# Kernel tuning notes

Hardware: AMD Instinct MI355X
Metric: run time of the kernel (lower is better)

Reference implementation:

```python
import jax, jax.numpy as jnp
import numpy as np


def setup_inputs() -> dict:
    key = jax.random.key(0)
    ks = jax.random.split(key, 5)
    B, C, H, W = 16, 512, 32, 32
    n_heads, d_k = 4, 128
    return {
        "x": jax.random.normal(ks[0], (B, C, H, W), dtype=jnp.float32),
        "w_proj": jax.random.normal(ks[1], (3 * n_heads * d_k, C), dtype=jnp.float32) * (1.0 / np.sqrt(C)),
        "b_proj": jax.random.normal(ks[2], (3 * n_heads * d_k,), dtype=jnp.float32) * 0.01,
        "w_out": jax.random.normal(ks[3], (C, n_heads * d_k), dtype=jnp.float32) * (1.0 / np.sqrt(n_heads * d_k)),
        "b_out": jax.random.normal(ks[4], (C,), dtype=jnp.float32) * 0.01,
        "n_heads": n_heads,
    }


def reference(x, w_proj, b_proj, w_out, b_out, n_heads):
    B, C, H, W = x.shape
    seq = H * W
    d_k = (w_proj.shape[0] // 3) // n_heads
    scale = d_k ** -0.5

    xs = x.reshape(B, C, seq).transpose(0, 2, 1)          # [B, seq, C]
    qkv = xs @ w_proj.T + b_proj                           # [B, seq, 3*H*d_k]
    qkv = qkv.reshape(B, seq, n_heads, 3 * d_k)
    q, k, v = jnp.split(qkv, 3, axis=-1)                   # each [B, seq, H, d_k]

    attn = jnp.einsum('bihd,bjhd->bijh', q, k) * scale     # [B, seq, seq, H]
    # NOTE: softmax over the QUERY axis (dim=1), faithful to the source quirk.
    attn = jax.nn.softmax(attn, axis=1)

    res = jnp.einsum('bijh,bjhd->bihd', attn, v)           # [B, seq, H, d_k]
    res = res.reshape(B, seq, n_heads * d_k)
    res = res @ w_out.T + b_out + xs                       # residual add
    return res.transpose(0, 2, 1).reshape(B, C, H, W)
```

## Files before the change

kernel.cpp:

```cpp
#include <hip/hip_runtime.h>
#include <hip/hip_bf16.h>
#include <math.h>

#define B_    16
#define CIN   512
#define SEQ   1024
#define NH    4
#define DK    128
#define OUT3  1536
#define SCALE 0.08838834764831845f

typedef __attribute__((ext_vector_type(8))) __bf16 bf16x8;
typedef __attribute__((ext_vector_type(4))) float f32x4;

#define MFMA(a, b, c) __builtin_amdgcn_mfma_f32_16x16x32_bf16((a), (b), (c), 0, 0, 0)

__device__ __forceinline__ ushort f2bf(float f) {
    __hip_bfloat16 h = __float2bfloat16(f);
    return *(ushort*)&h;
}
__device__ __forceinline__ uint pk2(float a, float b) {
    return (uint)f2bf(a) | ((uint)f2bf(b) << 16);
}

__global__ __launch_bounds__(256) void transpose_cast_kernel(
    const float* __restrict__ x, ushort* __restrict__ xt)
{
    __shared__ ushort t[64 * 66];
    const int tid = threadIdx.x;
    const int i0 = blockIdx.x * 64, c0 = blockIdx.y * 64, b = blockIdx.z;

    #pragma unroll
    for (int l = 0; l < 4; ++l) {
        int idx = tid + l * 256;
        int c = idx >> 4, i4 = (idx & 15) << 2;
        float4 v = *(const float4*)&x[((size_t)b * CIN + c0 + c) * SEQ + i0 + i4];
        t[(i4 + 0) * 66 + c] = f2bf(v.x);
        t[(i4 + 1) * 66 + c] = f2bf(v.y);
        t[(i4 + 2) * 66 + c] = f2bf(v.z);
        t[(i4 + 3) * 66 + c] = f2bf(v.w);
    }
    __syncthreads();
    #pragma unroll
    for (int l = 0; l < 4; ++l) {
        int idx = tid + l * 256;
        int i = idx >> 4, c4 = (idx & 15) << 2;
        uint2 p;
        p.x = *(const uint*)&t[i * 66 + c4];
        p.y = *(const uint*)&t[i * 66 + c4 + 2];
        *(uint2*)&xt[((size_t)b * SEQ + i0 + i) * CIN + c0 + c4] = p;
    }
}

__global__ __launch_bounds__(256) void qkv_kernel(
    const float* __restrict__ w, const float* __restrict__ bias,
    const ushort* __restrict__ xt,
    ushort* __restrict__ qb, ushort* __restrict__ kb, ushort* __restrict__ vtb)
{
    __shared__ ushort lds_w[128 * 40];
    __shared__ ushort lds_x[128 * 40];
    const int tid = threadIdx.x;
    const int lane = tid & 63, wv = tid >> 6;
    const int l15 = lane & 15, l4 = lane >> 4;
    const int wm = wv >> 1, wn = wv & 1;
    const int o0 = blockIdx.x * 128, i0 = blockIdx.y * 128, b = blockIdx.z;

    f32x4 acc[4][4] = {};
    for (int c0 = 0; c0 < CIN; c0 += 32) {
        __syncthreads();
        #pragma unroll
        for (int l = 0; l < 4; ++l) {
            int idx = tid + l * 256;
            int o = idx >> 3, cq = (idx & 7) << 2;
            float4 v = *(const float4*)&w[(size_t)(o0 + o) * CIN + c0 + cq];
            uint2 p; p.x = pk2(v.x, v.y); p.y = pk2(v.z, v.w);
            *(uint2*)&lds_w[o * 40 + cq] = p;
        }
        #pragma unroll
        for (int l = 0; l < 2; ++l) {
            int idx = tid + l * 256;
            int i = idx >> 2, cq = (idx & 3) << 3;
            *(uint4*)&lds_x[i * 40 + cq] =
                *(const uint4*)&xt[((size_t)b * SEQ + i0 + i) * CIN + c0 + cq];
        }
        __syncthreads();
        bf16x8 af[4], bfr[4];
        #pragma unroll
        for (int m = 0; m < 4; ++m)
            af[m] = *(const bf16x8*)&lds_w[(wm * 64 + m * 16 + l15) * 40 + (l4 << 3)];
        #pragma unroll
        for (int n = 0; n < 4; ++n)
            bfr[n] = *(const bf16x8*)&lds_x[(wn * 64 + n * 16 + l15) * 40 + (l4 << 3)];
        #pragma unroll
        for (int m = 0; m < 4; ++m)
            #pragma unroll
            for (int n = 0; n < 4; ++n)
                acc[m][n] = MFMA(af[m], bfr[n], acc[m][n]);
    }
    const int h = o0 / 384, which = (o0 % 384) / 128;
    const int bh = b * NH + h;
    #pragma unroll
    for (int m = 0; m < 4; ++m) {
        const int d0 = wm * 64 + m * 16 + (l4 << 2);
        float bia[4];
        #pragma unroll
        for (int r = 0; r < 4; ++r) bia[r] = bias[o0 + d0 + r];
        #pragma unroll
        for (int n = 0; n < 4; ++n) {
            const int i = i0 + wn * 64 + n * 16 + l15;
            float v0 = acc[m][n][0] + bia[0], v1 = acc[m][n][1] + bia[1];
            float v2 = acc[m][n][2] + bia[2], v3 = acc[m][n][3] + bia[3];
            if (which == 2) {
                vtb[((size_t)bh * DK + d0 + 0) * SEQ + i] = f2bf(v0);
                vtb[((size_t)bh * DK + d0 + 1) * SEQ + i] = f2bf(v1);
                vtb[((size_t)bh * DK + d0 + 2) * SEQ + i] = f2bf(v2);
                vtb[((size_t)bh * DK + d0 + 3) * SEQ + i] = f2bf(v3);
            } else {
                ushort* dst = (which == 0) ? qb : kb;
                uint2 p; p.x = pk2(v0, v1); p.y = pk2(v2, v3);
                *(uint2*)&dst[((size_t)bh * SEQ + i) * DK + d0] = p;
            }
        }
    }
}

__global__ __launch_bounds__(256) void stats_kernel(
    const ushort* __restrict__ qb, const ushort* __restrict__ kb,
    float* __restrict__ mstat, float* __restrict__ rstat)
{
    __shared__ ushort lds_q[64 * 136];
    const int tid = threadIdx.x;
    const int lane = tid & 63, wv = tid >> 6;
    const int l15 = lane & 15, l4 = lane >> 4;
    const int bh = blockIdx.y;
    const int j0 = blockIdx.x * 128 + wv * 32;
    const ushort* kbase = kb + (size_t)bh * SEQ * DK;
    const ushort* qbase = qb + (size_t)bh * SEQ * DK;

    bf16x8 kf[2][4];
    #pragma unroll
    for (int m = 0; m < 2; ++m)
        #pragma unroll
        for (int ks = 0; ks < 4; ++ks)
            kf[m][ks] = *(const bf16x8*)&kbase[(size_t)(j0 + m * 16 + l15) * DK
                                               + ks * 32 + (l4 << 3)];
    float mm[2][4], ss[2][4];
    #pragma unroll
    for (int m = 0; m < 2; ++m)
        #pragma unroll
        for (int r = 0; r < 4; ++r) { mm[m][r] = -1e30f; ss[m][r] = 0.0f; }

    for (int it = 0; it < SEQ / 64; ++it) {
        __syncthreads();
        #pragma unroll
        for (int l = 0; l < 4; ++l) {
            int idx = tid + l * 256;
            int i = idx >> 4, dq = (idx & 15) << 3;
            *(uint4*)&lds_q[i * 136 + dq] =
                *(const uint4*)&qbase[(size_t)(it * 64 + i) * DK + dq];
        }
        __syncthreads();
        #pragma unroll
        for (int n = 0; n < 4; ++n) {
            f32x4 a0 = {}, a1 = {};
            #pragma unroll
            for (int ks = 0; ks < 4; ++ks) {
                bf16x8 bq = *(const bf16x8*)&lds_q[(n * 16 + l15) * 136
                                                   + ks * 32 + (l4 << 3)];
                a0 = MFMA(kf[0][ks], bq, a0);
                a1 = MFMA(kf[1][ks], bq, a1);
            }
            #pragma unroll
            for (int r = 0; r < 4; ++r) {
                float v0 = a0[r] * SCALE;
                float n0 = fmaxf(mm[0][r], v0);
                ss[0][r] = ss[0][r] * __expf(mm[0][r] - n0) + __expf(v0 - n0);
                mm[0][r] = n0;
                float v1 = a1[r] * SCALE;
                float n1 = fmaxf(mm[1][r], v1);
                ss[1][r] = ss[1][r] * __expf(mm[1][r] - n1) + __expf(v1 - n1);
                mm[1][r] = n1;
            }
        }
    }
    #pragma unroll
    for (int m = 0; m < 2; ++m)
        #pragma unroll
        for (int r = 0; r < 4; ++r) {
            float mv = mm[m][r], sv = ss[m][r];
            #pragma unroll
            for (int wmask = 1; wmask < 16; wmask <<= 1) {
                float mo = __shfl_xor(mv, wmask, 64);
                float so = __shfl_xor(sv, wmask, 64);
                float mn = fmaxf(mv, mo);
                sv = sv * __expf(mv - mn) + so * __expf(mo - mn);
                mv = mn;
            }
            if (l15 == 0) {
                int j = j0 + m * 16 + (l4 << 2) + r;
                mstat[(size_t)bh * SEQ + j] = mv;
                rstat[(size_t)bh * SEQ + j] = 1.0f / sv;
            }
        }
}

__global__ __launch_bounds__(256) void attn_kernel(
    const ushort* __restrict__ qb, const ushort* __restrict__ kb,
    const ushort* __restrict__ vtb,
    const float* __restrict__ mstat, const float* __restrict__ rstat,
    ushort* __restrict__ resb)
{
    __shared__ ushort lds_k[64 * 136];
    __shared__ ushort lds_vt[128 * 72];
    __shared__ ushort lds_p[64 * 72];
    const int tid = threadIdx.x;
    const int lane = tid & 63, wv = tid >> 6;
    const int l15 = lane & 15, l4 = lane >> 4;
    const int wj = wv & 1, wi = wv >> 1;
    const int bh = blockIdx.y, b = bh >> 2, h = bh & 3;
    const int i0 = blockIdx.x * 64;
    const ushort* qbase = qb + (size_t)bh * SEQ * DK;
    const ushort* kbase = kb + (size_t)bh * SEQ * DK;
    const ushort* vtbase = vtb + (size_t)bh * DK * SEQ;

    bf16x8 qf[2][4];
    #pragma unroll
    for (int n = 0; n < 2; ++n)
        #pragma unroll
        for (int ks = 0; ks < 4; ++ks)
            qf[n][ks] = *(const bf16x8*)&qbase[(size_t)(i0 + wi * 32 + n * 16 + l15) * DK
                                               + ks * 32 + (l4 << 3)];
    f32x4 oacc[2][4] = {};

    for (int jt = 0; jt < SEQ / 64; ++jt) {
        const int j0 = jt * 64;
        __syncthreads();
        #pragma unroll
        for (int l = 0; l < 4; ++l) {
            int idx = tid + l * 256;
            int j = idx >> 4, dq = (idx & 15) << 3;
            *(uint4*)&lds_k[j * 136 + dq] =
                *(const uint4*)&kbase[(size_t)(j0 + j) * DK + dq];
        }
        #pragma unroll
        for (int l = 0; l < 4; ++l) {
            int idx = tid + l * 256;
            int d = idx >> 3, jq = (idx & 7) << 3;
            *(uint4*)&lds_vt[d * 72 + jq] =
                *(const uint4*)&vtbase[(size_t)d * SEQ + j0 + jq];
        }
        __syncthreads();
        float mj[2][4], rj[2][4];
        #pragma unroll
        for (int m = 0; m < 2; ++m)
            #pragma unroll
            for (int r = 0; r < 4; ++r) {
                int j = j0 + wj * 32 + m * 16 + (l4 << 2) + r;
                mj[m][r] = mstat[(size_t)bh * SEQ + j];
                rj[m][r] = rstat[(size_t)bh * SEQ + j];
            }
        bf16x8 af[2][4];
        #pragma unroll
        for (int m = 0; m < 2; ++m)
            #pragma unroll
            for (int ks = 0; ks < 4; ++ks)
                af[m][ks] = *(const bf16x8*)&lds_k[(wj * 32 + m * 16 + l15) * 136
                                                   + ks * 32 + (l4 << 3)];
        #pragma unroll
        for (int m = 0; m < 2; ++m)
            #pragma unroll
            for (int n = 0; n < 2; ++n) {
                f32x4 s = {};
                #pragma unroll
                for (int ks = 0; ks < 4; ++ks)
                    s = MFMA(af[m][ks], qf[n][ks], s);
                const int i = wi * 32 + n * 16 + l15;
                float p0 = __expf(s[0] * SCALE - mj[m][0]) * rj[m][0];
                float p1 = __expf(s[1] * SCALE - mj[m][1]) * rj[m][1];
                float p2 = __expf(s[2] * SCALE - mj[m][2]) * rj[m][2];
                float p3 = __expf(s[3] * SCALE - mj[m][3]) * rj[m][3];
                uint2 pp; pp.x = pk2(p0, p1); pp.y = pk2(p2, p3);
                *(uint2*)&lds_p[i * 72 + wj * 32 + m * 16 + (l4 << 2)] = pp;
            }
        __syncthreads();
        #pragma unroll
        for (int ks = 0; ks < 2; ++ks) {
            bf16x8 va0 = *(const bf16x8*)&lds_vt[(wv * 32 + 0  + l15) * 72 + ks * 32 + (l4 << 3)];
            bf16x8 va1 = *(const bf16x8*)&lds_vt[(wv * 32 + 16 + l15) * 72 + ks * 32 + (l4 << 3)];
            #pragma unroll
            for (int n = 0; n < 4; ++n) {
                bf16x8 pb = *(const bf16x8*)&lds_p[(n * 16 + l15) * 72 + ks * 32 + (l4 << 3)];
                oacc[0][n] = MFMA(va0, pb, oacc[0][n]);
                oacc[1][n] = MFMA(va1, pb, oacc[1][n]);
            }
        }
    }
    #pragma unroll
    for (int m = 0; m < 2; ++m)
        #pragma unroll
        for (int n = 0; n < 4; ++n) {
            const int i = i0 + n * 16 + l15;
            const int d = wv * 32 + m * 16 + (l4 << 2);
            uint2 p;
            p.x = pk2(oacc[m][n][0], oacc[m][n][1]);
            p.y = pk2(oacc[m][n][2], oacc[m][n][3]);
            *(uint2*)&resb[((size_t)b * SEQ + i) * (NH * DK) + h * DK + d] = p;
        }
}

__global__ __launch_bounds__(256) void outproj_kernel(
    const ushort* __restrict__ resb, const float* __restrict__ wout,
    const float* __restrict__ bout, const float* __restrict__ x,
    float* __restrict__ out)
{
    __shared__ ushort lds_w[128 * 40];
    __shared__ ushort lds_r[128 * 40];
    const int tid = threadIdx.x;
    const int lane = tid & 63, wv = tid >> 6;
    const int l15 = lane & 15, l4 = lane >> 4;
    const int wm = wv >> 1, wn = wv & 1;
    const int i0 = blockIdx.x * 128, c0 = blockIdx.y * 128, b = blockIdx.z;

    f32x4 acc[4][4] = {};
    for (int k0 = 0; k0 < NH * DK; k0 += 32) {
        __syncthreads();
        #pragma unroll
        for (int l = 0; l < 4; ++l) {
            int idx = tid + l * 256;
            int c = idx >> 3, kq = (idx & 7) << 2;
            float4 v = *(const float4*)&wout[(size_t)(c0 + c) * (NH * DK) + k0 + kq];
            uint2 p; p.x = pk2(v.x, v.y); p.y = pk2(v.z, v.w);
            *(uint2*)&lds_w[c * 40 + kq] = p;
        }
        #pragma unroll
        for (int l = 0; l < 2; ++l) {
            int idx = tid + l * 256;
            int i = idx >> 2, kq = (idx & 3) << 3;
            *(uint4*)&lds_r[i * 40 + kq] =
                *(const uint4*)&resb[((size_t)b * SEQ + i0 + i) * (NH * DK) + k0 + kq];
        }
        __syncthreads();
        bf16x8 af[4], bfr[4];
        #pragma unroll
        for (int m = 0; m < 4; ++m)
            af[m] = *(const bf16x8*)&lds_w[(wm * 64 + m * 16 + l15) * 40 + (l4 << 3)];
        #pragma unroll
        for (int n = 0; n < 4; ++n)
            bfr[n] = *(const bf16x8*)&lds_r[(wn * 64 + n * 16 + l15) * 40 + (l4 << 3)];
        #pragma unroll
        for (int m = 0; m < 4; ++m)
            #pragma unroll
            for (int n = 0; n < 4; ++n)
                acc[m][n] = MFMA(af[m], bfr[n], acc[m][n]);
    }
    #pragma unroll
    for (int m = 0; m < 4; ++m) {
        const int cb = c0 + wm * 64 + m * 16 + (l4 << 2);
        float bia[4];
        #pragma unroll
        for (int r = 0; r < 4; ++r) bia[r] = bout[cb + r];
        #pragma unroll
        for (int n = 0; n < 4; ++n) {
            const int i = i0 + wn * 64 + n * 16 + l15;
            #pragma unroll
            for (int r = 0; r < 4; ++r) {
                size_t off = ((size_t)b * CIN + cb + r) * SEQ + i;
                out[off] = acc[m][n][r] + bia[r] + x[off];
            }
        }
    }
}

extern "C" void kernel_launch(void* const* d_in, const int* in_sizes, int n_in,
                              void* d_out, int out_size, void* d_ws, size_t ws_size,
                              hipStream_t stream) {
    const float* x      = (const float*)d_in[0];
    const float* w_proj = (const float*)d_in[1];
    const float* b_proj = (const float*)d_in[2];
    const float* w_out  = (const float*)d_in[3];
    const float* b_out  = (const float*)d_in[4];

    const size_t xtE  = (size_t)B_ * SEQ * CIN;
    const size_t qkE  = (size_t)B_ * NH * SEQ * DK;
    ushort* xt    = (ushort*)d_ws;
    ushort* qb    = xt + xtE;
    ushort* kb    = qb + qkE;
    ushort* vtb   = kb + qkE;
    float*  mstat = (float*)(vtb + qkE);
    float*  rstat = mstat + (size_t)B_ * NH * SEQ;
    ushort* resb  = (ushort*)(rstat + (size_t)B_ * NH * SEQ);
    float*  out   = (float*)d_out;

    transpose_cast_kernel<<<dim3(SEQ / 64, CIN / 64, B_), 256, 0, stream>>>(x, xt);
    qkv_kernel<<<dim3(OUT3 / 128, SEQ / 128, B_), 256, 0, stream>>>(
        w_proj, b_proj, xt, qb, kb, vtb);
    stats_kernel<<<dim3(SEQ / 128, B_ * NH), 256, 0, stream>>>(qb, kb, mstat, rstat);
    attn_kernel<<<dim3(SEQ / 64, B_ * NH), 256, 0, stream>>>(
        qb, kb, vtb, mstat, rstat, resb);
    outproj_kernel<<<dim3(SEQ / 128, CIN / 128, B_), 256, 0, stream>>>(
        resb, w_out, b_out, x, out);
}
```

Before: 283.3 us.

## Use direct global-to-LDS loads, XOR swizzle, XCD block remap, and pre-cast weights

Weights are cast to bf16 once in separate kernels, so the GEMM loops no longer convert fp32 each iteration. All tile loads go straight from global memory to LDS, with XOR-swizzled layouts replacing padded ones to avoid bank conflicts. Block indices are remapped so neighbouring tiles land on the same XCD for better L2 reuse. The stats kernel batches its online softmax update across four columns to cut exp calls. The projection weight buffer reuses the resb workspace before attention overwrites it, which depends on launch ordering.

```diff
diff --git a/kernel.cpp b/kernel.cpp
--- a/kernel.cpp
+++ b/kernel.cpp
@@ -21,6 +21,14 @@
 }
 __device__ __forceinline__ uint pk2(float a, float b) {
     return (uint)f2bf(a) | ((uint)f2bf(b) << 16);
+}
+__device__ __forceinline__ void g2l16(const ushort* g, ushort* l) {
+    __builtin_amdgcn_global_load_lds(
+        (const __attribute__((address_space(1))) unsigned int*)g,
+        (__attribute__((address_space(3))) unsigned int*)l, 16, 0, 0);
+}
+__device__ __forceinline__ int xcdswz(int bid, int nwg) {
+    return (bid & 7) * (nwg >> 3) + (bid >> 3);
 }
 
 __global__ __launch_bounds__(256) void transpose_cast_kernel(
@@ -52,50 +60,63 @@
     }
 }
 
+__global__ __launch_bounds__(256) void cast_kernel(
+    const float* __restrict__ src, ushort* __restrict__ dst, int n4)
+{
+    int idx = blockIdx.x * 256 + threadIdx.x;
+    if (idx < n4) {
+        float4 v = *(const float4*)&src[(size_t)idx * 4];
+        uint2 p; p.x = pk2(v.x, v.y); p.y = pk2(v.z, v.w);
+        *(uint2*)&dst[(size_t)idx * 4] = p;
+    }
+}
+
 __global__ __launch_bounds__(256) void qkv_kernel(
-    const float* __restrict__ w, const float* __restrict__ bias,
+    const ushort* __restrict__ wbf, const float* __restrict__ bias,
     const ushort* __restrict__ xt,
     ushort* __restrict__ qb, ushort* __restrict__ kb, ushort* __restrict__ vtb)
 {
-    __shared__ ushort lds_w[128 * 40];
-    __shared__ ushort lds_x[128 * 40];
+    __shared__ __attribute__((aligned(16))) ushort lds_a[128 * 32];
+    __shared__ __attribute__((aligned(16))) ushort lds_b[128 * 32];
     const int tid = threadIdx.x;
     const int lane = tid & 63, wv = tid >> 6;
     const int l15 = lane & 15, l4 = lane >> 4;
     const int wm = wv >> 1, wn = wv & 1;
-    const int o0 = blockIdx.x * 128, i0 = blockIdx.y * 128, b = blockIdx.z;
+    const int swz = xcdswz(blockIdx.x, 1536);
+    const int o0 = (swz % 12) * 128;
+    const int i0 = ((swz / 12) & 7) * 128;
+    const int b  = swz / 96;
 
     f32x4 acc[4][4] = {};
     for (int c0 = 0; c0 < CIN; c0 += 32) {
         __syncthreads();
         #pragma unroll
-        for (int l = 0; l < 4; ++l) {
-            int idx = tid + l * 256;
-            int o = idx >> 3, cq = (idx & 7) << 2;
-            float4 v = *(const float4*)&w[(size_t)(o0 + o) * CIN + c0 + cq];
-            uint2 p; p.x = pk2(v.x, v.y); p.y = pk2(v.z, v.w);
-            *(uint2*)&lds_w[o * 40 + cq] = p;
-        }
-        #pragma unroll
         for (int l = 0; l < 2; ++l) {
-            int idx = tid + l * 256;
-            int i = idx >> 2, cq = (idx & 3) << 3;
-            *(uint4*)&lds_x[i * 40 + cq] =
-                *(const uint4*)&xt[((size_t)b * SEQ + i0 + i) * CIN + c0 + cq];
-        }
-        __syncthreads();
-        bf16x8 af[4], bfr[4];
+            int chunk = l * 256 + tid;
+            int row = chunk >> 2, c = chunk & 3;
+            g2l16(&wbf[(size_t)(o0 + row) * CIN + c0 + (c << 3)],
+                  &lds_a[(size_t)(l * 256 + wv * 64) * 8]);
+        }
+        #pragma unroll
+        for (int l = 0; l < 2; ++l) {
+            int chunk = l * 256 + tid;
+            int row = chunk >> 2, c = chunk & 3;
+            g2l16(&xt[((size_t)b * SEQ + i0 + row) * CIN + c0 + (c << 3)],
+                  &lds_b[(size_t)(l * 256 + wv * 64) * 8]);
+        }
+        __syncthreads();
+        bf16x8 af[4], bfv[4];
         #pragma unroll
         for (int m = 0; m < 4; ++m)
-            af[m] = *(const bf16x8*)&lds_w[(wm * 64 + m * 16 + l15) * 40 + (l4 << 3)];
+            af[m] = *(const bf16x8*)&lds_a[(wm * 64 + m * 16 + l15) * 32 + (l4 << 3)];
         #pragma unroll
         for (int n = 0; n < 4; ++n)
-            bfr[n] = *(const bf16x8*)&lds_x[(wn * 64 + n * 16 + l15) * 40 + (l4 << 3)];
+            bfv[n] = *(const bf16x8*)&lds_b[(wn * 64 + n * 16 + l15) * 32 + (l4 << 3)];
         #pragma unroll
         for (int m = 0; m < 4; ++m)
             #pragma unroll
             for (int n = 0; n < 4; ++n)
-                acc[m][n] = MFMA(af[m], bfr[n], acc[m][n]);
+                acc[m][n] = MFMA(af[m], bfv[n], acc[m][n]);
     }
     const int h = o0 / 384, which = (o0 % 384) / 128;
     const int bh = b * NH + h;
@@ -128,12 +149,13 @@
     const ushort* __restrict__ qb, const ushort* __restrict__ kb,
     float* __restrict__ mstat, float* __restrict__ rstat)
 {
-    __shared__ ushort lds_q[64 * 136];
+    __shared__ __attribute__((aligned(16))) ushort lds_q[64 * 128];
     const int tid = threadIdx.x;
     const int lane = tid & 63, wv = tid >> 6;
     const int l15 = lane & 15, l4 = lane >> 4;
-    const int bh = blockIdx.y;
-    const int j0 = blockIdx.x * 128 + wv * 32;
+    const int swz = xcdswz(blockIdx.x, 512);
+    const int bh = swz >> 3;
+    const int j0 = (swz & 7) * 128 + wv * 32;
     const ushort* kbase = kb + (size_t)bh * SEQ * DK;
     const ushort* qbase = qb + (size_t)bh * SEQ * DK;
 
@@ -154,32 +176,46 @@
         __syncthreads();
         #pragma unroll
         for (int l = 0; l < 4; ++l) {
-            int idx = tid + l * 256;
-            int i = idx >> 4, dq = (idx & 15) << 3;
-            *(uint4*)&lds_q[i * 136 + dq] =
-                *(const uint4*)&qbase[(size_t)(it * 64 + i) * DK + dq];
-        }
-        __syncthreads();
+            int chunk = l * 256 + tid;
+            int row = chunk >> 4, c = chunk & 15;
+            g2l16(&qbase[(size_t)(it * 64 + row) * DK + ((c ^ (row & 7)) << 3)],
+                  &lds_q[(size_t)(l * 256 + wv * 64) * 8]);
+        }
+        __syncthreads();
+        f32x4 sa0[4], sa1[4];
         #pragma unroll
         for (int n = 0; n < 4; ++n) {
             f32x4 a0 = {}, a1 = {};
             #pragma unroll
             for (int ks = 0; ks < 4; ++ks) {
-                bf16x8 bq = *(const bf16x8*)&lds_q[(n * 16 + l15) * 136
-                                                   + ks * 32 + (l4 << 3)];
+                bf16x8 bq = *(const bf16x8*)&lds_q[(n * 16 + l15) * 128
+                                + ((((ks << 2) | l4) ^ (l15 & 7)) << 3)];
                 a0 = MFMA(kf[0][ks], bq, a0);
                 a1 = MFMA(kf[1][ks], bq, a1);
             }
-            #pragma unroll
-            for (int r = 0; r < 4; ++r) {
-                float v0 = a0[r] * SCALE;
-                float n0 = fmaxf(mm[0][r], v0);
-                ss[0][r] = ss[0][r] * __expf(mm[0][r] - n0) + __expf(v0 - n0);
-                mm[0][r] = n0;
-                float v1 = a1[r] * SCALE;
-                float n1 = fmaxf(mm[1][r], v1);
-                ss[1][r] = ss[1][r] * __expf(mm[1][r] - n1) + __expf(v1 - n1);
-                mm[1][r] = n1;
+            sa0[n] = a0; sa1[n] = a1;
+        }
+        #pragma unroll
+        for (int r = 0; r < 4; ++r) {
+            {
+                float v0 = sa0[0][r] * SCALE, v1 = sa0[1][r] * SCALE;
+                float v2 = sa0[2][r] * SCALE, v3 = sa0[3][r] * SCALE;
+                float tm = fmaxf(fmaxf(v0, v1), fmaxf(v2, v3));
+                float nm = fmaxf(mm[0][r], tm);
+                float s4 = __expf(v0 - nm) + __expf(v1 - nm)
+                         + __expf(v2 - nm) + __expf(v3 - nm);
+                ss[0][r] = ss[0][r] * __expf(mm[0][r] - nm) + s4;
+                mm[0][r] = nm;
+            }
+            {
+                float v0 = sa1[0][r] * SCALE, v1 = sa1[1][r] * SCALE;
+                float v2 = sa1[2][r] * SCALE, v3 = sa1[3][r] * SCALE;
+                float tm = fmaxf(fmaxf(v0, v1), fmaxf(v2, v3));
+                float nm = fmaxf(mm[1][r], tm);
+                float s4 = __expf(v0 - nm) + __expf(v1 - nm)
+                         + __expf(v2 - nm) + __expf(v3 - nm);
+                ss[1][r] = ss[1][r] * __expf(mm[1][r] - nm) + s4;
+                mm[1][r] = nm;
             }
         }
     }
@@ -210,15 +246,16 @@
     const float* __restrict__ mstat, const float* __restrict__ rstat,
     ushort* __restrict__ resb)
 {
-    __shared__ ushort lds_k[64 * 136];
-    __shared__ ushort lds_vt[128 * 72];
-    __shared__ ushort lds_p[64 * 72];
+    __shared__ __attribute__((aligned(16))) ushort lds_k[64 * 128];
+    __shared__ __attribute__((aligned(16))) ushort lds_vt[128 * 64];
+    __shared__ __attribute__((aligned(16))) ushort lds_p[64 * 72];
     const int tid = threadIdx.x;
     const int lane = tid & 63, wv = tid >> 6;
     const int l15 = lane & 15, l4 = lane >> 4;
     const int wj = wv & 1, wi = wv >> 1;
-    const int bh = blockIdx.y, b = bh >> 2, h = bh & 3;
-    const int i0 = blockIdx.x * 64;
+    const int swz = xcdswz(blockIdx.x, 1024);
+    const int bh = swz >> 4, b = bh >> 2, h = bh & 3;
+    const int i0 = (swz & 15) * 64;
     const ushort* qbase = qb + (size_t)bh * SEQ * DK;
     const ushort* kbase = kb + (size_t)bh * SEQ * DK;
     const ushort* vtbase = vtb + (size_t)bh * DK * SEQ;
@@ -237,17 +274,17 @@
         __syncthreads();
         #pragma unroll
         for (int l = 0; l < 4; ++l) {
-            int idx = tid + l * 256;
-            int j = idx >> 4, dq = (idx & 15) << 3;
-            *(uint4*)&lds_k[j * 136 + dq] =
-                *(const uint4*)&kbase[(size_t)(j0 + j) * DK + dq];
+            int chunk = l * 256 + tid;
+            int row = chunk >> 4, c = chunk & 15;
+            g2l16(&kbase[(size_t)(j0 + row) * DK + ((c ^ (row & 7)) << 3)],
+                  &lds_k[(size_t)(l * 256 + wv * 64) * 8]);
         }
         #pragma unroll
         for (int l = 0; l < 4; ++l) {
-            int idx = tid + l * 256;
-            int d = idx >> 3, jq = (idx & 7) << 3;
-            *(uint4*)&lds_vt[d * 72 + jq] =
-                *(const uint4*)&vtbase[(size_t)d * SEQ + j0 + jq];
+            int chunk = l * 256 + tid;
+            int row = chunk >> 3, c = chunk & 7;
+            g2l16(&vtbase[(size_t)row * SEQ + j0 + ((c ^ (row & 7)) << 3)],
+                  &lds_vt[(size_t)(l * 256 + wv * 64) * 8]);
         }
         __syncthreads();
         float mj[2][4], rj[2][4];
@@ -264,8 +301,8 @@
         for (int m = 0; m < 2; ++m)
             #pragma unroll
             for (int ks = 0; ks < 4; ++ks)
-                af[m][ks] = *(const bf16x8*)&lds_k[(wj * 32 + m * 16 + l15) * 136
-                                                   + ks * 32 + (l4 << 3)];
+                af[m][ks] = *(const bf16x8*)&lds_k[(wj * 32 + m * 16 + l15) * 128
+                                + ((((ks << 2) | l4) ^ (l15 & 7)) << 3)];
         #pragma unroll
         for (int m = 0; m < 2; ++m)
             #pragma unroll
@@ -285,11 +322,14 @@
         __syncthreads();
         #pragma unroll
         for (int ks = 0; ks < 2; ++ks) {
-            bf16x8 va0 = *(const bf16x8*)&lds_vt[(wv * 32 + 0  + l15) * 72 + ks * 32 + (l4 << 3)];
-            bf16x8 va1 = *(const bf16x8*)&lds_vt[(wv * 32 + 16 + l15) * 72 + ks * 32 + (l4 << 3)];
+            bf16x8 va0 = *(const bf16x8*)&lds_vt[(wv * 32 + l15) * 64
+                            + ((((ks << 2) | l4) ^ (l15 & 7)) << 3)];
+            bf16x8 va1 = *(const bf16x8*)&lds_vt[(wv * 32 + 16 + l15) * 64
+                            + ((((ks << 2) | l4) ^ (l15 & 7)) << 3)];
             #pragma unroll
             for (int n = 0; n < 4; ++n) {
-                bf16x8 pb = *(const bf16x8*)&lds_p[(n * 16 + l15) * 72 + ks * 32 + (l4 << 3)];
+                bf16x8 pb = *(const bf16x8*)&lds_p[(n * 16 + l15) * 72
+                                + ks * 32 + (l4 << 3)];
                 oacc[0][n] = MFMA(va0, pb, oacc[0][n]);
                 oacc[1][n] = MFMA(va1, pb, oacc[1][n]);
             }
@@ -309,49 +349,51 @@
 }
 
 __global__ __launch_bounds__(256) void outproj_kernel(
-    const ushort* __restrict__ resb, const float* __restrict__ wout,
+    const ushort* __restrict__ resb, const ushort* __restrict__ woutbf,
     const float* __restrict__ bout, const float* __restrict__ x,
     float* __restrict__ out)
 {
-    __shared__ ushort lds_w[128 * 40];
-    __shared__ ushort lds_r[128 * 40];
+    __shared__ __attribute__((aligned(16))) ushort lds_a[128 * 32];
+    __shared__ __attribute__((aligned(16))) ushort lds_b[128 * 32];
     const int tid = threadIdx.x;
     const int lane = tid & 63, wv = tid >> 6;
     const int l15 = lane & 15, l4 = lane >> 4;
     const int wm = wv >> 1, wn = wv & 1;
-    const int i0 = blockIdx.x * 128, c0 = blockIdx.y * 128, b = blockIdx.z;
+    const int swz = xcdswz(blockIdx.x, 512);
+    const int i0 = (swz & 7) * 128;
+    const int c0 = ((swz >> 3) & 3) * 128;
+    const int b  = swz >> 5;
 
     f32x4 acc[4][4] = {};
     for (int k0 = 0; k0 < NH * DK; k0 += 32) {
         __syncthreads();
         #pragma unroll
-        for (int l = 0; l < 4; ++l) {
-            int idx = tid + l * 256;
-            int c = idx >> 3, kq = (idx & 7) << 2;
-            float4 v = *(const float4*)&wout[(size_t)(c0 + c) * (NH * DK) + k0 + kq];
-            uint2 p; p.x = pk2(v.x, v.y); p.y = pk2(v.z, v.w);
-            *(uint2*)&lds_w[c * 40 + kq] = p;
-        }
-        #pragma unroll
         for (int l = 0; l < 2; ++l) {
-            int idx = tid + l * 256;
-            int i = idx >> 2, kq = (idx & 3) << 3;
-            *(uint4*)&lds_r[i * 40 + kq] =
-                *(const uint4*)&resb[((size_t)b * SEQ + i0 + i) * (NH * DK) + k0 + kq];
-        }
-        __syncthreads();
-        bf16x8 af[4], bfr[4];
+            int chunk = l * 256 + tid;
+            int row = chunk >> 2, c = chunk & 3;
+            g2l16(&woutbf[(size_t)(c0 + row) * (NH * DK) + k0 + (c << 3)],
+                  &lds_a[(size_t)(l * 256 + wv * 64) * 8]);
+        }
+        #pragma unroll
+        for (int l = 0; l < 2; ++l) {
+            int chunk = l * 256 + tid;
+            int row = chunk >> 2, c = chunk & 3;
+            g2l16(&resb[((size_t)b * SEQ + i0 + row) * (NH * DK) + k0 + (c << 3)],
+                  &lds_b[(size_t)(l * 256 + wv * 64) * 8]);
+        }
+        __syncthreads();
+        bf16x8 af[4], bfv[4];
         #pragma unroll
         for (int m = 0; m < 4; ++m)
-            af[m] = *(const bf16x8*)&lds_w[(wm * 64 + m * 16 + l15) * 40 + (l4 << 3)];
+            af[m] = *(const bf16x8*)&lds_a[(wm * 64 + m * 16 + l15) * 32 + (l4 << 3)];
         #pragma unroll
         for (int n = 0; n < 4; ++n)
-            bfr[n] = *(const bf16x8*)&lds_r[(wn * 64 + n * 16 + l15) * 40 + (l4 << 3)];
+            bfv[n] = *(const bf16x8*)&lds_b[(wn * 64 + n * 16 + l15) * 32 + (l4 << 3)];
         #pragma unroll
         for (int m = 0; m < 4; ++m)
             #pragma unroll
             for (int n = 0; n < 4; ++n)
-                acc[m][n] = MFMA(af[m], bfr[n], acc[m][n]);
+                acc[m][n] = MFMA(af[m], bfv[n], acc[m][n]);
     }
     #pragma unroll
     for (int m = 0; m < 4; ++m) {
@@ -380,8 +422,8 @@
     const float* w_out  = (const float*)d_in[3];
     const float* b_out  = (const float*)d_in[4];
 
-    const size_t xtE  = (size_t)B_ * SEQ * CIN;
-    const size_t qkE  = (size_t)B_ * NH * SEQ * DK;
+    const size_t xtE = (size_t)B_ * SEQ * CIN;
+    const size_t qkE = (size_t)B_ * NH * SEQ * DK;
     ushort* xt    = (ushort*)d_ws;
     ushort* qb    = xt + xtE;
     ushort* kb    = qb + qkE;
@@ -389,14 +431,15 @@
     float*  mstat = (float*)(vtb + qkE);
     float*  rstat = mstat + (size_t)B_ * NH * SEQ;
     ushort* resb  = (ushort*)(rstat + (size_t)B_ * NH * SEQ);
+    ushort* wobf  = resb + (size_t)B_ * SEQ * (NH * DK);
+    ushort* wpbf  = resb;
     float*  out   = (float*)d_out;
 
     transpose_cast_kernel<<<dim3(SEQ / 64, CIN / 64, B_), 256, 0, stream>>>(x, xt);
-    qkv_kernel<<<dim3(OUT3 / 128, SEQ / 128, B_), 256, 0, stream>>>(
-        w_proj, b_proj, xt, qb, kb, vtb);
-    stats_kernel<<<dim3(SEQ / 128, B_ * NH), 256, 0, stream>>>(qb, kb, mstat, rstat);
-    attn_kernel<<<dim3(SEQ / 64, B_ * NH), 256, 0, stream>>>(
-        qb, kb, vtb, mstat, rstat, resb);
-    outproj_kernel<<<dim3(SEQ / 128, CIN / 128, B_), 256, 0, stream>>>(
-        resb, w_out, b_out, x, out);
-}
+    cast_kernel<<<dim3(768), 256, 0, stream>>>(w_proj, wpbf, 196608);
+    cast_kernel<<<dim3(256), 256, 0, stream>>>(w_out, wobf, 65536);
+    qkv_kernel<<<dim3(1536), 256, 0, stream>>>(wpbf, b_proj, xt, qb, kb, vtb);
+    stats_kernel<<<dim3(512), 256, 0, stream>>>(qb, kb, mstat, rstat);
+    attn_kernel<<<dim3(1024), 256, 0, stream>>>(qb, kb, vtb, mstat, rstat, resb);
+    outproj_kernel<<<dim3(512), 256, 0, stream>>>(resb, wobf, b_out, x, out);
+}
```

Measured after the change: 259.7 us. 8.3% less time.
